# Kernel tuning notes

Hardware: AMD Instinct MI355X
Metric: run time of the kernel (lower is better)

Reference implementation:

```python
import jax, jax.numpy as jnp
import numpy as np

N_SEQ = 250000
L = 40
C_IN = 20
K = 4
D = 32
N_BAGS = 100
SEQ_PER_BAG = N_SEQ // N_BAGS


def _param(key, shape):
    # matches torch init: normal(0, sqrt(1/prod(shape)))
    return jax.random.normal(key, shape, dtype=jnp.float32) * np.sqrt(1.0 / np.prod(shape))


def setup_inputs() -> dict:
    key = jax.random.key(0)
    ks = jax.random.split(key, 16)
    inp = {
        "x": jax.random.normal(ks[0], (N_SEQ, L, C_IN), dtype=jnp.float32),
        # equal-size bags: 100 bags of 2500 sequences (sum == N_SEQ)
        "n_per_bag": jnp.full((N_BAGS,), SEQ_PER_BAG, dtype=jnp.int32),
        # CNN: two conv1d layers, kernel shape (K, in, out) for 'NWC'/'WIO'
        "conv1_w": _param(ks[1], (K, C_IN, D)), "conv1_b": jnp.zeros((D,), jnp.float32),
        "conv2_w": _param(ks[2], (K, D, D)),    "conv2_b": jnp.zeros((D,), jnp.float32),
        # attention MLP: 32->32->32->1
        "att_w1": _param(ks[3], (D, D)), "att_b1": jnp.zeros((D,), jnp.float32),
        "att_w2": _param(ks[4], (D, D)), "att_b2": jnp.zeros((D,), jnp.float32),
        "att_w3": _param(ks[5], (D, 1)), "att_b3": jnp.zeros((1,), jnp.float32),
        # output net A: 32->32->21, output net B: 32->32->40
        "outA_w1": _param(ks[6], (D, D)),  "outA_b1": jnp.zeros((D,), jnp.float32),
        "outA_w2": _param(ks[7], (D, 21)), "outA_b2": jnp.zeros((21,), jnp.float32),
        "outB_w1": _param(ks[8], (D, D)),  "outB_b1": jnp.zeros((D,), jnp.float32),
        "outB_w2": _param(ks[9], (D, 40)), "outB_b2": jnp.zeros((40,), jnp.float32),
    }
    return inp


def _conv1d_nwc(x, w, b):
    # x: (N, L, Cin), w: (K, Cin, Cout) -> (N, L-K+1, Cout), VALID padding
    return jax.lax.conv_general_dilated(
        x, w, window_strides=(1,), padding="VALID",
        dimension_numbers=("NWC", "WIO", "NWC")) + b


def _forward(x, n_per_bag, conv1_w, conv1_b, conv2_w, conv2_b,
             att_w1, att_b1, att_w2, att_b2, att_w3, att_b3,
             outA_w1, outA_b1, outA_w2, outA_b2,
             outB_w1, outB_b1, outB_w2, outB_b2):
    selu = jax.nn.selu
    # --- sequence embedding CNN (dropout = identity in eval) ---
    h = selu(_conv1d_nwc(x, conv1_w, conv1_b))          # (N, L-3, D)
    h = selu(_conv1d_nwc(h, conv2_w, conv2_b))          # (N, L-6, D)
    seq_embed = h.max(axis=1)                           # (N, D)
    # --- attention scores ---
    a = selu(seq_embed @ att_w1 + att_b1)
    a = selu(a @ att_w2 + att_b2)
    scores = (a @ att_w3 + att_b3)[:, 0]                # (N,)
    # --- per-bag segment softmax + weighted-sum pooling ---
    seg = jnp.repeat(jnp.arange(N_BAGS, dtype=jnp.int32), np.asarray(n_per_bag),
                     total_repeat_length=seq_embed.shape[0])
    seg_max = jax.ops.segment_max(scores, seg, num_segments=N_BAGS)
    e = jnp.exp(scores - seg_max[seg])
    denom = jax.ops.segment_sum(e, seg, num_segments=N_BAGS)
    w = e / denom[seg]                                  # (N,)
    pooled = jax.ops.segment_sum(seq_embed * w[:, None], seg,
                                 num_segments=N_BAGS)   # (N_BAGS, D)
    # --- output networks (n_layers=2: one hidden SELU layer + final, then sigmoid) ---
    pa = jax.nn.sigmoid(selu(pooled @ outA_w1 + outA_b1) @ outA_w2 + outA_b2)
    pb = jax.nn.sigmoid(selu(pooled @ outB_w1 + outB_b1) @ outB_w2 + outB_b2)
    return pa, pb


def reference(x, n_per_bag, conv1_w, conv1_b, conv2_w, conv2_b,
              att_w1, att_b1, att_w2, att_b2, att_w3, att_b3,
              outA_w1, outA_b1, outA_w2, outA_b2,
              outB_w1, outB_b1, outB_w2, outB_b2):
    return _forward(x, n_per_bag, conv1_w, conv1_b, conv2_w, conv2_b,
                    att_w1, att_b1, att_w2, att_b2, att_w3, att_b3,
                    outA_w1, outA_b1, outA_w2, outA_b2,
                    outB_w1, outB_b1, outB_w2, outB_b2)
```

## Files before the change

kernel.cpp:

```cpp
#include <hip/hip_runtime.h>

#define N_SEQ 250000
#define LSEQ  40
#define CIN   20
#define KW    4
#define DCH   32
#define L1    37
#define L2    34
#define N_BAGS 100
#define SPB   2500
#define S_BLK 4
#define NTHR  256
#define R1    (S_BLK * L1)
#define R2    (S_BLK * L2)
#define T1C   5
#define T2C   5
#define H1S   36

typedef _Float16 f16;
typedef _Float16 f16x8 __attribute__((ext_vector_type(8)));
typedef _Float16 f16x4 __attribute__((ext_vector_type(4)));
typedef float    f32x16 __attribute__((ext_vector_type(16)));

__device__ __forceinline__ float selu_f(float x) {
  float e = 1.6732632423543772f * (__expf(x) - 1.0f);
  return 1.0507009873554805f * ((x > 0.0f) ? x : e);
}

__global__ __launch_bounds__(256) void prep_kernel(
    const float* __restrict__ w1, const float* __restrict__ w2,
    const float* __restrict__ aw1, const float* __restrict__ aw2,
    f16* __restrict__ w1T, f16* __restrict__ w2T,
    float* __restrict__ aw1T, float* __restrict__ aw2T)
{
  const int tid = threadIdx.x;
  for (int i = tid; i < 32 * 80; i += 256) {
    const int n = i / 80, k = i - n * 80;
    w1T[i] = (f16)w1[k * 32 + n];
  }
  for (int i = tid; i < 32 * 128; i += 256) {
    const int n = i >> 7, k = i & 127;
    w2T[i] = (f16)w2[k * 32 + n];
  }
  for (int i = tid; i < 1024; i += 256) {
    const int d = i >> 5, c = i & 31;
    aw1T[i] = aw1[c * 32 + d];
    aw2T[i] = aw2[c * 32 + d];
  }
}

__global__ __launch_bounds__(NTHR, 4) void seq_kernel(
    const float* __restrict__ x,
    const f16*  __restrict__ w1T, const float* __restrict__ b1,
    const f16*  __restrict__ w2T, const float* __restrict__ b2,
    const float* __restrict__ aw1T, const float* __restrict__ ab1,
    const float* __restrict__ aw2T, const float* __restrict__ ab2,
    const float* __restrict__ aw3, const float* __restrict__ ab3,
    f16* __restrict__ se_out, float* __restrict__ sc_out)
{
  __shared__ __align__(16) f16 xs[S_BLK * LSEQ * CIN];
  __shared__ __align__(16) f16 h1[R1 * H1S];
  __shared__ float pt[T2C][2][DCH];

  const int tid  = threadIdx.x;
  const int lane = tid & 63;
  const int wave = tid >> 6;
  const int m    = lane & 31;
  const int half = lane >> 5;
  const int seq0 = blockIdx.x * S_BLK;

  {
    const float4* xg = (const float4*)(x + (size_t)blockIdx.x * (S_BLK * LSEQ * CIN));
    for (int i = tid; i < S_BLK * LSEQ * CIN / 4; i += NTHR) {
      const float4 v = xg[i];
      f16x4 h; h[0] = (f16)v.x; h[1] = (f16)v.y; h[2] = (f16)v.z; h[3] = (f16)v.w;
      *(f16x4*)&xs[i * 4] = h;
    }
  }

  f16x8 bf1[5];
  {
    const f16x8* w1t8 = (const f16x8*)w1T;
    #pragma unroll
    for (int kc = 0; kc < 5; kc++) bf1[kc] = w1t8[m * 10 + kc * 2 + half];
  }
  const float b1v = b1[m];
  __syncthreads();

  for (int tile = wave; tile < T1C; tile += 4) {
    const unsigned r  = tile * 32 + m;
    const unsigned rc = (r < R1) ? r : (R1 - 1);
    const unsigned s  = rc / L1, l = rc - s * L1;
    const f16* arow = &xs[(s * LSEQ + l) * CIN];
    f32x16 acc;
    #pragma unroll
    for (int i = 0; i < 16; i++) acc[i] = b1v;
    #pragma unroll
    for (int kc = 0; kc < 5; kc++) {
      const int e = kc * 16 + half * 8;
      const f16x4 p0 = *(const f16x4*)(arow + e);
      const f16x4 p1 = *(const f16x4*)(arow + e + 4);
      const f16x8 a = __builtin_shufflevector(p0, p1, 0, 1, 2, 3, 4, 5, 6, 7);
      acc = __builtin_amdgcn_mfma_f32_32x32x16_f16(a, bf1[kc], acc, 0, 0, 0);
    }
    #pragma unroll
    for (int reg = 0; reg < 16; reg++) {
      const int rr = tile * 32 + (reg & 3) + 8 * (reg >> 2) + 4 * half;
      if (rr < R1) h1[rr * H1S + m] = (f16)selu_f(acc[reg]);
    }
  }

  f16x8 bf2[8];
  {
    const f16x8* w2t8 = (const f16x8*)w2T;
    #pragma unroll
    for (int kc = 0; kc < 8; kc++) bf2[kc] = w2t8[m * 16 + kc * 2 + half];
  }
  const float b2v = b2[m];
  __syncthreads();

  for (int tile = wave; tile < T2C; tile += 4) {
    const unsigned r  = tile * 32 + m;
    const unsigned rc = (r < R2) ? r : (R2 - 1);
    const unsigned s  = rc / L2, l = rc - s * L2;
    const f16* abase = &h1[(s * L1 + l) * H1S];
    f32x16 acc;
    #pragma unroll
    for (int i = 0; i < 16; i++) acc[i] = b2v;
    #pragma unroll
    for (int kc = 0; kc < 8; kc++) {
      const int e = (kc >> 1) * H1S + (kc & 1) * 16 + half * 8;
      const f16x4 p0 = *(const f16x4*)(abase + e);
      const f16x4 p1 = *(const f16x4*)(abase + e + 4);
      const f16x8 a = __builtin_shufflevector(p0, p1, 0, 1, 2, 3, 4, 5, 6, 7);
      acc = __builtin_amdgcn_mfma_f32_32x32x16_f16(a, bf2[kc], acc, 0, 0, 0);
    }
    const int s0  = (tile * 32 * 241) >> 13;
    const int bnd = (s0 + 1) * L2;
    float mx0 = -3.4e38f, mx1 = -3.4e38f;
    #pragma unroll
    for (int reg = 0; reg < 16; reg++) {
      int rr = tile * 32 + (reg & 3) + 8 * (reg >> 2) + 4 * half;
      if (rr > R2 - 1) rr = R2 - 1;
      if (rr < bnd) mx0 = fmaxf(mx0, acc[reg]);
      else          mx1 = fmaxf(mx1, acc[reg]);
    }
    mx0 = fmaxf(mx0, __shfl_xor(mx0, 32, 64));
    mx1 = fmaxf(mx1, __shfl_xor(mx1, 32, 64));
    if (half == 0) { pt[tile][0][m] = mx0; pt[tile][1][m] = mx1; }
  }
  __syncthreads();

  if (tid < S_BLK * DCH) {
    const int s = tid >> 5, d = tid & 31;
    const int tA = (s * L2) >> 5;
    const int tB = (s * L2 + L2 - 1) >> 5;
    const int sA = ((tA << 5) * 241) >> 13;
    const int sB = ((tB << 5) * 241) >> 13;
    const float mx = fmaxf(pt[tA][(s == sA) ? 0 : 1][d],
                           pt[tB][(s == sB) ? 0 : 1][d]);
    const float sv = selu_f(mx);
    se_out[(size_t)seq0 * DCH + tid] = (f16)sv;

    const float4* wt1 = (const float4*)aw1T;
    float a = ab1[d];
    #pragma unroll
    for (int c4 = 0; c4 < 8; c4++) {
      const float4 w = wt1[d * 8 + c4];
      a = fmaf(__shfl(sv, c4 * 4 + 0, 32), w.x, a);
      a = fmaf(__shfl(sv, c4 * 4 + 1, 32), w.y, a);
      a = fmaf(__shfl(sv, c4 * 4 + 2, 32), w.z, a);
      a = fmaf(__shfl(sv, c4 * 4 + 3, 32), w.w, a);
    }
    const float av = selu_f(a);

    const float4* wt2 = (const float4*)aw2T;
    float a2 = ab2[d];
    #pragma unroll
    for (int c4 = 0; c4 < 8; c4++) {
      const float4 w = wt2[d * 8 + c4];
      a2 = fmaf(__shfl(av, c4 * 4 + 0, 32), w.x, a2);
      a2 = fmaf(__shfl(av, c4 * 4 + 1, 32), w.y, a2);
      a2 = fmaf(__shfl(av, c4 * 4 + 2, 32), w.z, a2);
      a2 = fmaf(__shfl(av, c4 * 4 + 3, 32), w.w, a2);
    }
    float p = selu_f(a2) * aw3[d];
    #pragma unroll
    for (int off = 16; off > 0; off >>= 1) p += __shfl_xor(p, off, 32);
    if (d == 0) sc_out[seq0 + s] = p + ab3[0];
  }
}

__global__ __launch_bounds__(256) void bag_kernel(
    const f16* __restrict__ se, const float* __restrict__ sc,
    const float* __restrict__ aw1, const float* __restrict__ ab1,
    const float* __restrict__ aw2, const float* __restrict__ ab2,
    const float* __restrict__ bw1, const float* __restrict__ bb1,
    const float* __restrict__ bw2, const float* __restrict__ bb2,
    float* __restrict__ out)
{
  const int bag = blockIdx.x, tid = threadIdx.x;
  const size_t base = (size_t)bag * SPB;

  __shared__ float pr[4][33];
  __shared__ float red[33];
  __shared__ float pool[DCH], hA[DCH], hB[DCH];

  float m = -3.4e38f;
  for (int i = tid; i < SPB; i += 256) m = fmaxf(m, sc[base + i]);
  #pragma unroll
  for (int off = 32; off > 0; off >>= 1) m = fmaxf(m, __shfl_xor(m, off, 64));
  if ((tid & 63) == 0) pr[tid >> 6][0] = m;
  __syncthreads();
  const float bagmax = fmaxf(fmaxf(pr[0][0], pr[1][0]), fmaxf(pr[2][0], pr[3][0]));
  __syncthreads();

  float acc[33];
  #pragma unroll
  for (int d = 0; d < 33; d++) acc[d] = 0.0f;
  for (int i = tid; i < SPB; i += 256) {
    const float e = __expf(sc[base + i] - bagmax);
    acc[32] += e;
    const f16* sr = &se[(base + i) * DCH];
    #pragma unroll
    for (int q = 0; q < 8; q++) {
      const f16x4 v = *(const f16x4*)(sr + q * 4);
      #pragma unroll
      for (int j = 0; j < 4; j++) acc[q * 4 + j] = fmaf(e, (float)v[j], acc[q * 4 + j]);
    }
  }
  #pragma unroll
  for (int d = 0; d < 33; d++) {
    float v = acc[d];
    #pragma unroll
    for (int off = 32; off > 0; off >>= 1) v += __shfl_xor(v, off, 64);
    if ((tid & 63) == 0) pr[tid >> 6][d] = v;
  }
  __syncthreads();
  if (tid < 33) red[tid] = pr[0][tid] + pr[1][tid] + pr[2][tid] + pr[3][tid];
  __syncthreads();
  if (tid < DCH) pool[tid] = red[tid] / red[32];
  __syncthreads();

  if (tid < DCH) {
    float a = ab1[tid], b = bb1[tid];
    #pragma unroll
    for (int c = 0; c < DCH; c++) {
      a = fmaf(pool[c], aw1[c * DCH + tid], a);
      b = fmaf(pool[c], bw1[c * DCH + tid], b);
    }
    hA[tid] = selu_f(a);
    hB[tid] = selu_f(b);
  }
  __syncthreads();

  if (tid < 21) {
    float v = ab2[tid];
    #pragma unroll
    for (int d = 0; d < DCH; d++) v = fmaf(hA[d], aw2[d * 21 + tid], v);
    out[bag * 21 + tid] = 1.0f / (1.0f + __expf(-v));
  } else if (tid >= 32 && tid < 72) {
    const int j = tid - 32;
    float v = bb2[j];
    #pragma unroll
    for (int d = 0; d < DCH; d++) v = fmaf(hB[d], bw2[d * 40 + j], v);
    out[N_BAGS * 21 + bag * 40 + j] = 1.0f / (1.0f + __expf(-v));
  }
}

extern "C" void kernel_launch(void* const* d_in, const int* in_sizes, int n_in,
                              void* d_out, int out_size, void* d_ws, size_t ws_size,
                              hipStream_t stream)
{
  const float* x    = (const float*)d_in[0];
  const float* c1w  = (const float*)d_in[2];
  const float* c1b  = (const float*)d_in[3];
  const float* c2w  = (const float*)d_in[4];
  const float* c2b  = (const float*)d_in[5];
  const float* aw1  = (const float*)d_in[6];
  const float* ab1  = (const float*)d_in[7];
  const float* aw2  = (const float*)d_in[8];
  const float* ab2  = (const float*)d_in[9];
  const float* aw3  = (const float*)d_in[10];
  const float* ab3  = (const float*)d_in[11];
  const float* oaw1 = (const float*)d_in[12];
  const float* oab1 = (const float*)d_in[13];
  const float* oaw2 = (const float*)d_in[14];
  const float* oab2 = (const float*)d_in[15];
  const float* obw1 = (const float*)d_in[16];
  const float* obb1 = (const float*)d_in[17];
  const float* obw2 = (const float*)d_in[18];
  const float* obb2 = (const float*)d_in[19];
  float* out = (float*)d_out;

  char* ws = (char*)d_ws;
  f16*   seh  = (f16*)ws;
  float* sc   = (float*)(ws + (size_t)16000000);
  f16*   w1T  = (f16*)(ws + (size_t)17000000);
  f16*   w2T  = w1T + 2560 + 2560;
  float* aw1T = (float*)(ws + (size_t)17000000 + 32768);
  float* aw2T = aw1T + 1024;

  prep_kernel<<<1, 256, 0, stream>>>(c1w, c2w, aw1, aw2, w1T, w2T, aw1T, aw2T);
  seq_kernel<<<N_SEQ / S_BLK, NTHR, 0, stream>>>(x, w1T, c1b, w2T, c2b,
                                                 aw1T, ab1, aw2T, ab2, aw3, ab3,
                                                 seh, sc);
  bag_kernel<<<N_BAGS, 256, 0, stream>>>(seh, sc, oaw1, oab1, oaw2, oab2,
                                         obw1, obb1, obw2, obb2, out);
}
```

Baseline: 1.441 ms.

## Map one sequence per wavefront and drop block-level syncs in seq kernel

Restructures seq_kernel so each wavefront owns one sequence end to end: it loads its own input, runs both conv MFMA stages over two row tiles, takes the max in registers and computes the attention MLP with readlane broadcasts. This removes the block-wide __syncthreads, the shared partial-max table and the cross-tile sequence-boundary logic, and it moves the conv2 bias add to after the max. The cost is more MFMA work on padded rows (the second tile of each stage is mostly clamped duplicate rows) and all 64 lanes now run the MLP tail where fewer did before. The h1 row stride grows to 40 so the conv2 A operand can be read with single 16-byte loads.

```diff
diff --git a/kernel.cpp b/kernel.cpp
--- a/kernel.cpp
+++ b/kernel.cpp
@@ -9,13 +9,9 @@
 #define L2    34
 #define N_BAGS 100
 #define SPB   2500
-#define S_BLK 4
 #define NTHR  256
-#define R1    (S_BLK * L1)
-#define R2    (S_BLK * L2)
-#define T1C   5
-#define T2C   5
-#define H1S   36
+#define WPB   4
+#define H1S   40
 
 typedef _Float16 f16;
 typedef _Float16 f16x8 __attribute__((ext_vector_type(8)));
@@ -25,6 +21,10 @@
 __device__ __forceinline__ float selu_f(float x) {
   float e = 1.6732632423543772f * (__expf(x) - 1.0f);
   return 1.0507009873554805f * ((x > 0.0f) ? x : e);
+}
+
+__device__ __forceinline__ float lane_bcast(float v, int srclane) {
+  return __int_as_float(__builtin_amdgcn_readlane(__float_as_int(v), srclane));
 }
 
 __global__ __launch_bounds__(256) void prep_kernel(
@@ -58,23 +58,28 @@
     const float* __restrict__ aw3, const float* __restrict__ ab3,
     f16* __restrict__ se_out, float* __restrict__ sc_out)
 {
-  __shared__ __align__(16) f16 xs[S_BLK * LSEQ * CIN];
-  __shared__ __align__(16) f16 h1[R1 * H1S];
-  __shared__ float pt[T2C][2][DCH];
+  __shared__ __align__(16) f16 xs[WPB][LSEQ * CIN];
+  __shared__ __align__(16) f16 h1[WPB][L1 * H1S];
 
   const int tid  = threadIdx.x;
   const int lane = tid & 63;
   const int wave = tid >> 6;
   const int m    = lane & 31;
   const int half = lane >> 5;
-  const int seq0 = blockIdx.x * S_BLK;
+  const int seq  = blockIdx.x * WPB + wave;
+
+  f16* xw  = xs[wave];
+  f16* h1w = h1[wave];
 
   {
-    const float4* xg = (const float4*)(x + (size_t)blockIdx.x * (S_BLK * LSEQ * CIN));
-    for (int i = tid; i < S_BLK * LSEQ * CIN / 4; i += NTHR) {
-      const float4 v = xg[i];
-      f16x4 h; h[0] = (f16)v.x; h[1] = (f16)v.y; h[2] = (f16)v.z; h[3] = (f16)v.w;
-      *(f16x4*)&xs[i * 4] = h;
+    const float4* xg = (const float4*)(x + (size_t)seq * (LSEQ * CIN));
+    for (int i = lane; i < 100; i += 64) {
+      const float4 v0 = xg[2 * i];
+      const float4 v1 = xg[2 * i + 1];
+      f16x8 h;
+      h[0] = (f16)v0.x; h[1] = (f16)v0.y; h[2] = (f16)v0.z; h[3] = (f16)v0.w;
+      h[4] = (f16)v1.x; h[5] = (f16)v1.y; h[6] = (f16)v1.z; h[7] = (f16)v1.w;
+      *(f16x8*)&xw[i * 8] = h;
     }
   }
 
@@ -85,13 +90,11 @@
     for (int kc = 0; kc < 5; kc++) bf1[kc] = w1t8[m * 10 + kc * 2 + half];
   }
   const float b1v = b1[m];
-  __syncthreads();
-
-  for (int tile = wave; tile < T1C; tile += 4) {
-    const unsigned r  = tile * 32 + m;
-    const unsigned rc = (r < R1) ? r : (R1 - 1);
-    const unsigned s  = rc / L1, l = rc - s * L1;
-    const f16* arow = &xs[(s * LSEQ + l) * CIN];
+
+  #pragma unroll
+  for (int tile = 0; tile < 2; tile++) {
+    const int l = tile ? min(32 + m, L1 - 1) : m;
+    const f16* arow = &xw[l * CIN];
     f32x16 acc;
     #pragma unroll
     for (int i = 0; i < 16; i++) acc[i] = b1v;
@@ -103,10 +106,20 @@
       const f16x8 a = __builtin_shufflevector(p0, p1, 0, 1, 2, 3, 4, 5, 6, 7);
       acc = __builtin_amdgcn_mfma_f32_32x32x16_f16(a, bf1[kc], acc, 0, 0, 0);
     }
-    #pragma unroll
-    for (int reg = 0; reg < 16; reg++) {
-      const int rr = tile * 32 + (reg & 3) + 8 * (reg >> 2) + 4 * half;
-      if (rr < R1) h1[rr * H1S + m] = (f16)selu_f(acc[reg]);
+    if (tile == 0) {
+      #pragma unroll
+      for (int reg = 0; reg < 16; reg++) {
+        const int rr = (reg & 3) + 8 * (reg >> 2) + 4 * half;
+        h1w[rr * H1S + m] = (f16)selu_f(acc[reg]);
+      }
+    } else {
+      if (half == 0) {
+        #pragma unroll
+        for (int reg = 0; reg < 4; reg++)
+          h1w[(32 + reg) * H1S + m] = (f16)selu_f(acc[reg]);
+      } else {
+        h1w[36 * H1S + m] = (f16)selu_f(acc[0]);
+      }
     }
   }
 
@@ -117,77 +130,59 @@
     for (int kc = 0; kc < 8; kc++) bf2[kc] = w2t8[m * 16 + kc * 2 + half];
   }
   const float b2v = b2[m];
-  __syncthreads();
-
-  for (int tile = wave; tile < T2C; tile += 4) {
-    const unsigned r  = tile * 32 + m;
-    const unsigned rc = (r < R2) ? r : (R2 - 1);
-    const unsigned s  = rc / L2, l = rc - s * L2;
-    const f16* abase = &h1[(s * L1 + l) * H1S];
+
+  float mx = -3.4e38f;
+  #pragma unroll
+  for (int tile = 0; tile < 2; tile++) {
+    const int l = tile ? min(32 + m, L2 - 1) : m;
+    const f16* abase = &h1w[l * H1S];
     f32x16 acc;
     #pragma unroll
-    for (int i = 0; i < 16; i++) acc[i] = b2v;
+    for (int i = 0; i < 16; i++) acc[i] = 0.0f;
     #pragma unroll
     for (int kc = 0; kc < 8; kc++) {
       const int e = (kc >> 1) * H1S + (kc & 1) * 16 + half * 8;
-      const f16x4 p0 = *(const f16x4*)(abase + e);
-      const f16x4 p1 = *(const f16x4*)(abase + e + 4);
-      const f16x8 a = __builtin_shufflevector(p0, p1, 0, 1, 2, 3, 4, 5, 6, 7);
+      const f16x8 a = *(const f16x8*)(abase + e);
       acc = __builtin_amdgcn_mfma_f32_32x32x16_f16(a, bf2[kc], acc, 0, 0, 0);
     }
-    const int s0  = (tile * 32 * 241) >> 13;
-    const int bnd = (s0 + 1) * L2;
-    float mx0 = -3.4e38f, mx1 = -3.4e38f;
-    #pragma unroll
-    for (int reg = 0; reg < 16; reg++) {
-      int rr = tile * 32 + (reg & 3) + 8 * (reg >> 2) + 4 * half;
-      if (rr > R2 - 1) rr = R2 - 1;
-      if (rr < bnd) mx0 = fmaxf(mx0, acc[reg]);
-      else          mx1 = fmaxf(mx1, acc[reg]);
-    }
-    mx0 = fmaxf(mx0, __shfl_xor(mx0, 32, 64));
-    mx1 = fmaxf(mx1, __shfl_xor(mx1, 32, 64));
-    if (half == 0) { pt[tile][0][m] = mx0; pt[tile][1][m] = mx1; }
-  }
-  __syncthreads();
-
-  if (tid < S_BLK * DCH) {
-    const int s = tid >> 5, d = tid & 31;
-    const int tA = (s * L2) >> 5;
-    const int tB = (s * L2 + L2 - 1) >> 5;
-    const int sA = ((tA << 5) * 241) >> 13;
-    const int sB = ((tB << 5) * 241) >> 13;
-    const float mx = fmaxf(pt[tA][(s == sA) ? 0 : 1][d],
-                           pt[tB][(s == sB) ? 0 : 1][d]);
-    const float sv = selu_f(mx);
-    se_out[(size_t)seq0 * DCH + tid] = (f16)sv;
-
+    if (tile == 0) {
+      #pragma unroll
+      for (int reg = 0; reg < 16; reg++) mx = fmaxf(mx, acc[reg]);
+    } else if (half == 0) {
+      mx = fmaxf(mx, fmaxf(acc[0], acc[1]));
+    }
+  }
+  mx = fmaxf(mx, __shfl_xor(mx, 32, 64));
+  const float sv = selu_f(mx + b2v);
+  if (half == 0) se_out[(size_t)seq * DCH + m] = (f16)sv;
+
+  {
     const float4* wt1 = (const float4*)aw1T;
-    float a = ab1[d];
+    float a = ab1[m];
     #pragma unroll
     for (int c4 = 0; c4 < 8; c4++) {
-      const float4 w = wt1[d * 8 + c4];
-      a = fmaf(__shfl(sv, c4 * 4 + 0, 32), w.x, a);
-      a = fmaf(__shfl(sv, c4 * 4 + 1, 32), w.y, a);
-      a = fmaf(__shfl(sv, c4 * 4 + 2, 32), w.z, a);
-      a = fmaf(__shfl(sv, c4 * 4 + 3, 32), w.w, a);
+      const float4 w = wt1[m * 8 + c4];
+      a = fmaf(lane_bcast(sv, c4 * 4 + 0), w.x, a);
+      a = fmaf(lane_bcast(sv, c4 * 4 + 1), w.y, a);
+      a = fmaf(lane_bcast(sv, c4 * 4 + 2), w.z, a);
+      a = fmaf(lane_bcast(sv, c4 * 4 + 3), w.w, a);
     }
     const float av = selu_f(a);
 
     const float4* wt2 = (const float4*)aw2T;
-    float a2 = ab2[d];
+    float a2 = ab2[m];
     #pragma unroll
     for (int c4 = 0; c4 < 8; c4++) {
-      const float4 w = wt2[d * 8 + c4];
-      a2 = fmaf(__shfl(av, c4 * 4 + 0, 32), w.x, a2);
-      a2 = fmaf(__shfl(av, c4 * 4 + 1, 32), w.y, a2);
-      a2 = fmaf(__shfl(av, c4 * 4 + 2, 32), w.z, a2);
-      a2 = fmaf(__shfl(av, c4 * 4 + 3, 32), w.w, a2);
-    }
-    float p = selu_f(a2) * aw3[d];
+      const float4 w = wt2[m * 8 + c4];
+      a2 = fmaf(lane_bcast(av, c4 * 4 + 0), w.x, a2);
+      a2 = fmaf(lane_bcast(av, c4 * 4 + 1), w.y, a2);
+      a2 = fmaf(lane_bcast(av, c4 * 4 + 2), w.z, a2);
+      a2 = fmaf(lane_bcast(av, c4 * 4 + 3), w.w, a2);
+    }
+    float p = selu_f(a2) * aw3[m];
     #pragma unroll
     for (int off = 16; off > 0; off >>= 1) p += __shfl_xor(p, off, 32);
-    if (d == 0) sc_out[seq0 + s] = p + ab3[0];
+    if (lane == 0) sc_out[seq] = p + ab3[0];
   }
 }
 
@@ -302,9 +297,9 @@
   float* aw2T = aw1T + 1024;
 
   prep_kernel<<<1, 256, 0, stream>>>(c1w, c2w, aw1, aw2, w1T, w2T, aw1T, aw2T);
-  seq_kernel<<<N_SEQ / S_BLK, NTHR, 0, stream>>>(x, w1T, c1b, w2T, c2b,
-                                                 aw1T, ab1, aw2T, ab2, aw3, ab3,
-                                                 seh, sc);
+  seq_kernel<<<N_SEQ / WPB, NTHR, 0, stream>>>(x, w1T, c1b, w2T, c2b,
+                                               aw1T, ab1, aw2T, ab2, aw3, ab3,
+                                               seh, sc);
   bag_kernel<<<N_BAGS, 256, 0, stream>>>(seh, sc, oaw1, oab1, oaw2, oab2,
                                          obw1, obb1, obw2, obb2, out);
 }
```

Result: slower. 1.602 ms (+11.2%).
